# Performance work log

Hardware: AMD Instinct MI355X
Metric: run time of the kernel (lower is better)

## Reference

```python
import jax, jax.numpy as jnp
import numpy as np

B, S, D, H = 2, 2048, 1024, 16
DK = D // H

def setup_inputs() -> dict:
    key = jax.random.key(0)
    ks = jax.random.split(key, 11)
    s = 1.0 / np.sqrt(D)
    inp = {
        'q': jax.random.normal(ks[0], (B, S, D), jnp.float32),
        'k': jax.random.normal(ks[1], (B, S, D), jnp.float32),
        'v': jax.random.normal(ks[2], (B, S, D), jnp.float32),
        'mask': jnp.tril(jnp.ones((S, S), jnp.bool_))[None, None],  # [1,1,S,S] causal
        'w_q': jax.random.normal(ks[3], (D, D), jnp.float32) * s,
        'b_q': jax.random.normal(ks[4], (D,), jnp.float32) * s,
        'w_k': jax.random.normal(ks[5], (D, D), jnp.float32) * s,
        'b_k': jax.random.normal(ks[6], (D,), jnp.float32) * s,
        'w_v': jax.random.normal(ks[7], (D, D), jnp.float32) * s,
        'b_v': jax.random.normal(ks[8], (D,), jnp.float32) * s,
        'w_o': jax.random.normal(ks[9], (D, D), jnp.float32) * s,
        'b_o': jax.random.normal(ks[10], (D,), jnp.float32) * s,
    }
    return inp

def reference(q, k, v, mask, w_q, b_q, w_k, b_k, w_v, b_v, w_o, b_o):
    # Linear projections (torch Linear: x @ W^T + b)
    qh = (q @ w_q.T + b_q).reshape(B, S, H, DK).transpose(0, 2, 1, 3)  # [B,H,S,DK]
    kh = (k @ w_k.T + b_k).reshape(B, S, H, DK).transpose(0, 2, 1, 3)
    vh = (v @ w_v.T + b_v).reshape(B, S, H, DK).transpose(0, 2, 1, 3)
    scores = jnp.einsum('bhqd,bhkd->bhqk', qh, kh) / jnp.sqrt(jnp.float32(DK))
    scores = jnp.where(mask, scores, jnp.float32(-jnp.inf))
    attn = jax.nn.softmax(scores, axis=-1)  # dropout p=0.0 -> identity
    out = jnp.einsum('bhqk,bhkd->bhqd', attn, vh)
    out = out.transpose(0, 2, 1, 3).reshape(B, S, D)
    return out @ w_o.T + b_o
```

## Files before the change

### kernel.cpp

```cpp
#include <hip/hip_runtime.h>
#include <hip/hip_bf16.h>

typedef __bf16 bf16_t;
typedef __bf16 bf16x4 __attribute__((ext_vector_type(4)));
typedef __bf16 bf16x8 __attribute__((ext_vector_type(8)));
typedef float f32x4 __attribute__((ext_vector_type(4)));

#define B_ 2
#define S_ 2048
#define D_ 1024
#define H_ 16
#define DK_ 64
#define M_ (B_ * S_)

__device__ __forceinline__ f32x4 mfma16(bf16x8 a, bf16x8 b, f32x4 c) {
  return __builtin_amdgcn_mfma_f32_16x16x32_bf16(a, b, c, 0, 0, 0);
}

__device__ __forceinline__ void async_load16(const bf16_t* g, bf16_t* l) {
  __builtin_amdgcn_global_load_lds(
      (const __attribute__((address_space(1))) void*)g,
      (__attribute__((address_space(3))) void*)l, 16, 0, 0);
}


__global__ void cvt_all(const float* __restrict__ q, const float* __restrict__ k,
                        const float* __restrict__ v, const float* __restrict__ w0,
                        const float* __restrict__ w1, const float* __restrict__ w2,
                        const float* __restrict__ w3, bf16_t* __restrict__ qb,
                        bf16_t* __restrict__ kb, bf16_t* __restrict__ vb,
                        bf16_t* __restrict__ o0, bf16_t* __restrict__ o1,
                        bf16_t* __restrict__ o2, bf16_t* __restrict__ o3) {
  const int y = blockIdx.y;
  if (y >= 3 && blockIdx.x >= 512) return;
  const float* src;
  bf16_t* dst;
  float sc = 1.0f;
  switch (y) {
    case 0: src = q; dst = qb; break;
    case 1: src = k; dst = kb; break;
    case 2: src = v; dst = vb; break;
    case 3: src = w0; dst = o0; sc = 0.125f; break;
    case 4: src = w1; dst = o1; break;
    case 5: src = w2; dst = o2; break;
    default: src = w3; dst = o3; break;
  }
  long i = ((long)blockIdx.x * blockDim.x + threadIdx.x) * 8;
  const float4* s4 = (const float4*)(src + i);
  float4 a = s4[0], b = s4[1];
  bf16x8 o;
  o[0] = (bf16_t)(a.x * sc); o[1] = (bf16_t)(a.y * sc);
  o[2] = (bf16_t)(a.z * sc); o[3] = (bf16_t)(a.w * sc);
  o[4] = (bf16_t)(b.x * sc); o[5] = (bf16_t)(b.y * sc);
  o[6] = (bf16_t)(b.z * sc); o[7] = (bf16_t)(b.w * sc);
  *(bf16x8*)(dst + i) = o;
}


template <int MODE>
__device__ __forceinline__ void gemm_core(const bf16_t* __restrict__ A,
                                          const bf16_t* __restrict__ W,
                                          const float* __restrict__ bias,
                                          float bscale, void* __restrict__ Cv) {
  constexpr int N = 1024, K = 1024;
  __shared__ bf16_t As[128 * 32];
  __shared__ bf16_t Bs[128 * 32];
  const int tid = threadIdx.x;
  const int wave = tid >> 6, lane = tid & 63;
  const int quad = lane >> 4, l15 = lane & 15;
  const int wm = wave >> 1, wn = wave & 1;
  const int bm = blockIdx.y * 128, bn = blockIdx.x * 128;

  f32x4 acc[4][4] = {};

  const int srow = wave * 32 + (lane >> 2);
  const int scol = (lane & 3) * 8;
  const bf16_t* ag = A + (long)(bm + srow) * K + scol;
  const bf16_t* bg = W + (long)(bn + srow) * K + scol;
  bf16_t* asl0 = &As[(wave * 32) * 32];
  bf16_t* asl1 = &As[(wave * 32 + 16) * 32];
  bf16_t* bsl0 = &Bs[(wave * 32) * 32];
  bf16_t* bsl1 = &Bs[(wave * 32 + 16) * 32];

  for (int kk = 0; kk < K; kk += 32) {
    __syncthreads();
    async_load16(ag + kk, asl0);
    async_load16(ag + kk + 16L * K, asl1);
    async_load16(bg + kk, bsl0);
    async_load16(bg + kk + 16L * K, bsl1);
    __syncthreads();
    bf16x8 af[4], bf[4];
#pragma unroll
    for (int i = 0; i < 4; ++i)
      af[i] = *(const bf16x8*)&As[(wm * 64 + i * 16 + l15) * 32 + quad * 8];
#pragma unroll
    for (int i = 0; i < 4; ++i)
      bf[i] = *(const bf16x8*)&Bs[(wn * 64 + i * 16 + l15) * 32 + quad * 8];
#pragma unroll
    for (int mi = 0; mi < 4; ++mi)
#pragma unroll
      for (int ni = 0; ni < 4; ++ni)
        acc[mi][ni] = mfma16(af[mi], bf[ni], acc[mi][ni]);
  }

#pragma unroll
  for (int mi = 0; mi < 4; ++mi) {
#pragma unroll
    for (int ni = 0; ni < 4; ++ni) {
      const int col = bn + wn * 64 + ni * 16 + l15;
      const float bsv = bias[col] * bscale;
      f32x4 v = acc[mi][ni];
      const int row0 = bm + wm * 64 + mi * 16 + quad * 4;
      if (MODE == 3) {
        float* C = (float*)Cv;
#pragma unroll
        for (int r = 0; r < 4; ++r)
          C[(long)(row0 + r) * N + col] = v[r] + bsv;
      } else if (MODE == 1) {
        bf16_t* C = (bf16_t*)Cv;
        const int hh = col >> 6, dk = col & 63;
        const int bq = row0 >> 11, s0 = row0 & 2047;
        bf16_t* base = C + (((long)bq * H_ + hh) * S_ + s0) * DK_ + dk;
#pragma unroll
        for (int r = 0; r < 4; ++r)
          base[(long)r * DK_] = (bf16_t)(v[r] + bsv);
      } else {
        bf16_t* C = (bf16_t*)Cv;
        const int hh = col >> 6, dk = col & 63;
        const int bq = row0 >> 11, s0 = row0 & 2047;
        bf16x4 pk;
#pragma unroll
        for (int r = 0; r < 4; ++r) pk[r] = (bf16_t)(v[r] + bsv);
        *(bf16x4*)(C + (((long)bq * H_ + hh) * DK_ + dk) * S_ + s0) = pk;
      }
    }
  }
}

__global__ __launch_bounds__(256) void gemm_qkv(
    const bf16_t* __restrict__ qb, const bf16_t* __restrict__ kb,
    const bf16_t* __restrict__ vb, const bf16_t* __restrict__ wq,
    const bf16_t* __restrict__ wk, const bf16_t* __restrict__ wv,
    const float* __restrict__ biq, const float* __restrict__ bik,
    const float* __restrict__ biv, bf16_t* __restrict__ Qh,
    bf16_t* __restrict__ Kh, bf16_t* __restrict__ Vt) {
  if (blockIdx.z == 0)
    gemm_core<1>(qb, wq, biq, 0.125f, Qh);
  else if (blockIdx.z == 1)
    gemm_core<1>(kb, wk, bik, 1.0f, Kh);
  else
    gemm_core<2>(vb, wv, biv, 1.0f, Vt);
}

__global__ __launch_bounds__(256) void gemm_out64(
    const bf16_t* __restrict__ AO, const bf16_t* __restrict__ wo,
    const float* __restrict__ bo, float* __restrict__ out) {
  constexpr int N = 1024, K = 1024;
  __shared__ bf16_t As[64 * 32];
  __shared__ bf16_t Bs[128 * 32];
  const int tid = threadIdx.x;
  const int wave = tid >> 6, lane = tid & 63;
  const int quad = lane >> 4, l15 = lane & 15;
  const int wm = wave >> 1, wn = wave & 1;
  const int bm = blockIdx.y * 64, bn = blockIdx.x * 128;

  f32x4 acc[2][4] = {};

  const int srow = lane >> 2;
  const int scol = (lane & 3) * 8;
  const bf16_t* ag = AO + (long)(bm + wave * 16 + srow) * K + scol;
  const bf16_t* bg = wo + (long)(bn + wave * 32 + srow) * K + scol;
  bf16_t* asl = &As[(wave * 16) * 32];
  bf16_t* bsl0 = &Bs[(wave * 32) * 32];
  bf16_t* bsl1 = &Bs[(wave * 32 + 16) * 32];

  for (int kk = 0; kk < K; kk += 32) {
    __syncthreads();
    async_load16(ag + kk, asl);
    async_load16(bg + kk, bsl0);
    async_load16(bg + kk + 16L * K, bsl1);
    __syncthreads();
    bf16x8 af[2], bf[4];
#pragma unroll
    for (int i = 0; i < 2; ++i)
      af[i] = *(const bf16x8*)&As[(wm * 32 + i * 16 + l15) * 32 + quad * 8];
#pragma unroll
    for (int i = 0; i < 4; ++i)
      bf[i] = *(const bf16x8*)&Bs[(wn * 64 + i * 16 + l15) * 32 + quad * 8];
#pragma unroll
    for (int mi = 0; mi < 2; ++mi)
#pragma unroll
      for (int ni = 0; ni < 4; ++ni)
        acc[mi][ni] = mfma16(af[mi], bf[ni], acc[mi][ni]);
  }

#pragma unroll
  for (int mi = 0; mi < 2; ++mi) {
#pragma unroll
    for (int ni = 0; ni < 4; ++ni) {
      const int col = bn + wn * 64 + ni * 16 + l15;
      const float bsv = bo[col];
      f32x4 v = acc[mi][ni];
      const int row0 = bm + wm * 32 + mi * 16 + quad * 4;
#pragma unroll
      for (int r = 0; r < 4; ++r)
        out[(long)(row0 + r) * N + col] = v[r] + bsv;
    }
  }
}


__device__ __forceinline__ int swzK(int b) {
  return b ^ (((b >> 7) & 3) << 4) ^ (((b >> 10) & 1) << 6);
}
__device__ __forceinline__ int swzV(int b) {
  return b ^ (((b >> 7) & 7) << 4);
}

template <bool MASKED>
__device__ __forceinline__ void softmax_pa(const f32x4 st[4], float& l_i,
                                           bf16x8& pa0, bf16x8& pa1,
                                           const int qcol, const int quad) {
#pragma unroll
  for (int nb = 0; nb < 4; ++nb) {
    const int kvb = quad * 8 + (nb & 1) * 4 + (nb >> 1) * 32;
#pragma unroll
    for (int r = 0; r < 4; ++r) {
      float x = st[nb][r];
      if (MASKED && (kvb + r) > qcol) x = -30000.f;
      const float pv = __expf(x);
      l_i += pv;
      const bf16_t pb = (bf16_t)pv;
      const int idx = ((nb & 1) << 2) | r;
      if (nb < 2) pa0[idx] = pb;
      else        pa1[idx] = pb;
    }
  }
}

__global__ __launch_bounds__(256, 3) void flash_attn3(
    const bf16_t* __restrict__ Qh, const bf16_t* __restrict__ Kh,
    const bf16_t* __restrict__ Vt, bf16_t* __restrict__ Po,
    float* __restrict__ Pl) {
  const int bid = blockIdx.x;
  const int g = bid & 31;
  const int z = bid >> 5;
  const int i = z / 3, pi = z % 3;
  const int h = g & 15, b = g >> 4;
  const int tA = i, tB = 31 - i;
  const int tid = threadIdx.x, wave = tid >> 6, lane = tid & 63;
  const int quad = lane >> 4, l15 = lane & 15;
  const int qcol = wave * 16 + l15;
  const int prow = ((l15 >> 2) << 3) | (l15 & 3);

  __shared__ bf16_t Kls[2][64 * 64];
  __shared__ bf16_t Vls[2][64 * 64];

  const bf16_t* qhead = Qh + ((long)(b * H_ + h) * S_) * DK_;
  const bf16_t* khead = Kh + ((long)(b * H_ + h) * S_) * DK_;
  const bf16_t* vhead = Vt + ((long)(b * H_ + h) * DK_) * S_;

  int koffe[2], voffe[2], ldse[2];
#pragma unroll
  for (int c = 0; c < 2; ++c) {
    const int bb = c * 4096 + wave * 1024 + lane * 16;
    koffe[c] = swzK(bb) >> 1;
    const int vs = swzV(bb);
    voffe[c] = (vs >> 7) * S_ + ((vs & 127) >> 1);
    ldse[c] = c * 2048 + wave * 512;
  }

  int kro[4][2], vro[4][2];
#pragma unroll
  for (int nb = 0; nb < 4; ++nb) {
    const int krow = prow + (nb & 1) * 4 + (nb >> 1) * 32;
    const int vrow = nb * 16 + l15;
#pragma unroll
    for (int hh = 0; hh < 2; ++hh) {
      kro[nb][hh] = swzK(krow * 128 + quad * 16 + hh * 64) >> 1;
      vro[nb][hh] = swzV(vrow * 128 + quad * 16 + hh * 64) >> 1;
    }
  }

  const int qA = tA * 64 + wave * 16;
  const int qB = tB * 64 + wave * 16;
  const bf16_t* qpA = qhead + (long)(qA + l15) * DK_ + quad * 8;
  const bf16_t* qpB = qhead + (long)(qB + l15) * DK_ + quad * 8;
  const bf16x8 aqA0 = *(const bf16x8*)qpA;
  const bf16x8 aqA1 = *(const bf16x8*)(qpA + 32);
  const bf16x8 aqB0 = *(const bf16x8*)qpB;
  const bf16x8 aqB1 = *(const bf16x8*)(qpB + 32);

  f32x4 oA[4] = {}, oB[4] = {};
  float lA = 0.f, lB = 0.f;

  {
    const bf16_t* kt = khead + pi * (64 * DK_);
    const bf16_t* vt = vhead + pi * 64;
#pragma unroll
    for (int c = 0; c < 2; ++c) {
      async_load16(kt + koffe[c], &Kls[0][ldse[c]]);
      async_load16(vt + voffe[c], &Vls[0][ldse[c]]);
    }
  }

  int cur = 0;
  for (int j = pi; j <= tB; j += 3) {
    const bool pf = (j + 3 <= tB);
    if (pf) {
      const bf16_t* kt = khead + (j + 3) * (64 * DK_);
      const bf16_t* vt = vhead + (j + 3) * 64;
#pragma unroll
      for (int c = 0; c < 2; ++c) {
        async_load16(kt + koffe[c], &Kls[cur ^ 1][ldse[c]]);
        async_load16(vt + voffe[c], &Vls[cur ^ 1][ldse[c]]);
      }
      asm volatile("s_waitcnt vmcnt(4)" ::: "memory");
    } else {
      asm volatile("s_waitcnt vmcnt(0)" ::: "memory");
    }
    __builtin_amdgcn_sched_barrier(0);
    __builtin_amdgcn_s_barrier();
    __builtin_amdgcn_sched_barrier(0);

    const bf16_t* Kc = &Kls[cur][0];
    const bf16_t* Vc = &Vls[cur][0];

    bf16x8 k0[4], k1[4];
#pragma unroll
    for (int nb = 0; nb < 4; ++nb) {
      k0[nb] = *(const bf16x8*)&Kc[kro[nb][0]];
      k1[nb] = *(const bf16x8*)&Kc[kro[nb][1]];
    }

    bf16x8 paB0, paB1, paA0, paA1;
    {
      f32x4 stB[4];
#pragma unroll
      for (int nb = 0; nb < 4; ++nb) {
        f32x4 t = {};
        t = mfma16(k0[nb], aqB0, t);
        t = mfma16(k1[nb], aqB1, t);
        stB[nb] = t;
      }
      if (j == tB)
        softmax_pa<true>(stB, lB, paB0, paB1, qcol, quad);
      else
        softmax_pa<false>(stB, lB, paB0, paB1, qcol, quad);
    }
    const bool doA = (j <= tA);
    if (doA) {
      f32x4 stA[4];
#pragma unroll
      for (int nb = 0; nb < 4; ++nb) {
        f32x4 t = {};
        t = mfma16(k0[nb], aqA0, t);
        t = mfma16(k1[nb], aqA1, t);
        stA[nb] = t;
      }
      if (j == tA)
        softmax_pa<true>(stA, lA, paA0, paA1, qcol, quad);
      else
        softmax_pa<false>(stA, lA, paA0, paA1, qcol, quad);
    }

    bf16x8 v0[4], v1[4];
#pragma unroll
    for (int nb = 0; nb < 4; ++nb) {
      v0[nb] = *(const bf16x8*)&Vc[vro[nb][0]];
      v1[nb] = *(const bf16x8*)&Vc[vro[nb][1]];
    }
#pragma unroll
    for (int nb = 0; nb < 4; ++nb) {
      oB[nb] = mfma16(paB0, v0[nb], oB[nb]);
      oB[nb] = mfma16(paB1, v1[nb], oB[nb]);
    }
    if (doA) {
#pragma unroll
      for (int nb = 0; nb < 4; ++nb) {
        oA[nb] = mfma16(paA0, v0[nb], oA[nb]);
        oA[nb] = mfma16(paA1, v1[nb], oA[nb]);
      }
    }

    asm volatile("s_waitcnt lgkmcnt(0)" ::: "memory");
    __builtin_amdgcn_sched_barrier(0);
    __builtin_amdgcn_s_barrier();
    cur ^= 1;
  }

  lA += __shfl_xor(lA, 16, 64);
  lA += __shfl_xor(lA, 32, 64);
  lB += __shfl_xor(lB, 16, 64);
  lB += __shfl_xor(lB, 32, 64);

  bf16_t* po = Po + (long)pi * (M_ * D_);
  bf16_t* poA = po + (long)(b * S_ + qA + quad * 4) * D_ + h * DK_ + l15;
  bf16_t* poB = po + (long)(b * S_ + qB + quad * 4) * D_ + h * DK_ + l15;
#pragma unroll
  for (int r = 0; r < 4; ++r) {
#pragma unroll
    for (int nb = 0; nb < 4; ++nb) {
      poA[(long)r * D_ + nb * 16] = (bf16_t)oA[nb][r];
      poB[(long)r * D_ + nb * 16] = (bf16_t)oB[nb][r];
    }
  }

  if (quad == 0) {
    float* pl = Pl + (long)pi * (B_ * H_ * S_) + (long)(b * H_ + h) * S_;
    pl[qA + l15] = lA;
    pl[qB + l15] = lB;
  }
}


__global__ __launch_bounds__(256) void merge_po(const bf16_t* __restrict__ Po,
                                                const float* __restrict__ Pl,
                                                bf16_t* __restrict__ AO) {
  const long e = ((long)blockIdx.x * 256 + threadIdx.x) * 8;
  const int bs = (int)(e >> 10);
  const int d = (int)(e & 1023);
  const int h = d >> 6;
  const int b = bs >> 11, s = bs & 2047;
  const long lidx = ((long)(b * H_ + h)) * S_ + s;

  float acc[8] = {0.f, 0.f, 0.f, 0.f, 0.f, 0.f, 0.f, 0.f};
  float L = 0.f;
#pragma unroll
  for (int p = 0; p < 3; ++p) {
    bf16x8 x = *(const bf16x8*)(Po + (long)p * (M_ * D_) + e);
#pragma unroll
    for (int k = 0; k < 8; ++k) acc[k] += (float)x[k];
    L += Pl[(long)p * (B_ * H_ * S_) + lidx];
  }
  const float inv = 1.f / L;
  bf16x8 y;
#pragma unroll
  for (int k = 0; k < 8; ++k) y[k] = (bf16_t)(acc[k] * inv);
  *(bf16x8*)(AO + e) = y;
}


extern "C" void kernel_launch(void* const* d_in, const int* in_sizes, int n_in,
                              void* d_out, int out_size, void* d_ws, size_t ws_size,
                              hipStream_t stream) {
  const float* q = (const float*)d_in[0];
  const float* k = (const float*)d_in[1];
  const float* v = (const float*)d_in[2];
  const float* wq = (const float*)d_in[4];
  const float* bq = (const float*)d_in[5];
  const float* wk = (const float*)d_in[6];
  const float* bk = (const float*)d_in[7];
  const float* wv = (const float*)d_in[8];
  const float* bv = (const float*)d_in[9];
  const float* wo = (const float*)d_in[10];
  const float* bo = (const float*)d_in[11];
  float* out = (float*)d_out;

  char* ws = (char*)d_ws;
  const size_t MB = 1024 * 1024;
  bf16_t* Qh = (bf16_t*)(ws);
  bf16_t* Kh = (bf16_t*)(ws + 8 * MB);
  bf16_t* Vt = (bf16_t*)(ws + 16 * MB);
  bf16_t* AO = (bf16_t*)(ws + 24 * MB);
  bf16_t* qb = (bf16_t*)(ws + 32 * MB);
  bf16_t* kb = (bf16_t*)(ws + 40 * MB);
  bf16_t* vb = (bf16_t*)(ws + 48 * MB);
  bf16_t* wqb = (bf16_t*)(ws + 56 * MB);
  bf16_t* wkb = (bf16_t*)(ws + 58 * MB);
  bf16_t* wvb = (bf16_t*)(ws + 60 * MB);
  bf16_t* wob = (bf16_t*)(ws + 62 * MB);
  bf16_t* Po = (bf16_t*)(ws + 32 * MB);
  float* Pl = (float*)(ws + 56 * MB);

  cvt_all<<<dim3(2048, 7, 1), 256, 0, stream>>>(q, k, v, wq, wk, wv, wo, qb, kb,
                                                vb, wqb, wkb, wvb, wob);
  gemm_qkv<<<dim3(8, 32, 3), 256, 0, stream>>>(qb, kb, vb, wqb, wkb, wvb, bq, bk,
                                               bv, Qh, Kh, Vt);
  flash_attn3<<<dim3(1536, 1, 1), 256, 0, stream>>>(Qh, Kh, Vt, Po, Pl);
  merge_po<<<dim3(2048, 1, 1), 256, 0, stream>>>(Po, Pl, AO);
  gemm_out64<<<dim3(8, 64, 1), 256, 0, stream>>>(AO, wob, bo, out);
}
```

Measured before the change: 221.2 us.

## Double-buffer GEMM tiles with BK=64, swizzled LDS, and swapped grid order

Rewrites the QKV and output-projection GEMM main loops to use double-buffered LDS with a K-step of 64. The next tile is prefetched via async global-to-LDS loads while MFMAs run on the current one, and an XOR swizzle is applied to avoid LDS bank conflicts. The grid mapping is also swapped so consecutive blocks walk along M and reuse the same weight tile in cache. The change doubles LDS usage per block, which may reduce occupancy, and it relies on hand-tuned vmcnt waits.

```diff
diff --git a/kernel.cpp b/kernel.cpp
--- a/kernel.cpp
+++ b/kernel.cpp
@@ -57,50 +57,89 @@
 }
 
 
+__device__ __forceinline__ int swzG(int b) {
+  return b ^ (((b >> 7) & 7) << 4);
+}
+
+template <int NR>
+__device__ __forceinline__ void stage_tile(const bf16_t* g, bf16_t* lds,
+                                           const int* srcoff, int wave) {
+#pragma unroll
+  for (int rnd = 0; rnd < NR; ++rnd)
+    async_load16(g + srcoff[rnd], lds + rnd * 2048 + wave * 512);
+}
+
 template <int MODE>
 __device__ __forceinline__ void gemm_core(const bf16_t* __restrict__ A,
                                           const bf16_t* __restrict__ W,
                                           const float* __restrict__ bias,
                                           float bscale, void* __restrict__ Cv) {
   constexpr int N = 1024, K = 1024;
-  __shared__ bf16_t As[128 * 32];
-  __shared__ bf16_t Bs[128 * 32];
+  __shared__ bf16_t As[2][128 * 64];
+  __shared__ bf16_t Bs[2][128 * 64];
   const int tid = threadIdx.x;
   const int wave = tid >> 6, lane = tid & 63;
   const int quad = lane >> 4, l15 = lane & 15;
   const int wm = wave >> 1, wn = wave & 1;
-  const int bm = blockIdx.y * 128, bn = blockIdx.x * 128;
+  const int bm = blockIdx.x * 128, bn = blockIdx.y * 128;
 
   f32x4 acc[4][4] = {};
 
-  const int srow = wave * 32 + (lane >> 2);
-  const int scol = (lane & 3) * 8;
-  const bf16_t* ag = A + (long)(bm + srow) * K + scol;
-  const bf16_t* bg = W + (long)(bn + srow) * K + scol;
-  bf16_t* asl0 = &As[(wave * 32) * 32];
-  bf16_t* asl1 = &As[(wave * 32 + 16) * 32];
-  bf16_t* bsl0 = &Bs[(wave * 32) * 32];
-  bf16_t* bsl1 = &Bs[(wave * 32 + 16) * 32];
-
-  for (int kk = 0; kk < K; kk += 32) {
-    __syncthreads();
-    async_load16(ag + kk, asl0);
-    async_load16(ag + kk + 16L * K, asl1);
-    async_load16(bg + kk, bsl0);
-    async_load16(bg + kk + 16L * K, bsl1);
-    __syncthreads();
-    bf16x8 af[4], bf[4];
-#pragma unroll
-    for (int i = 0; i < 4; ++i)
-      af[i] = *(const bf16x8*)&As[(wm * 64 + i * 16 + l15) * 32 + quad * 8];
-#pragma unroll
-    for (int i = 0; i < 4; ++i)
-      bf[i] = *(const bf16x8*)&Bs[(wn * 64 + i * 16 + l15) * 32 + quad * 8];
-#pragma unroll
-    for (int mi = 0; mi < 4; ++mi)
-#pragma unroll
-      for (int ni = 0; ni < 4; ++ni)
-        acc[mi][ni] = mfma16(af[mi], bf[ni], acc[mi][ni]);
+  int srcoff[4];
+#pragma unroll
+  for (int rnd = 0; rnd < 4; ++rnd) {
+    const int bb = rnd * 4096 + tid * 16;
+    const int sb = swzG(bb);
+    srcoff[rnd] = (sb >> 7) * K + ((sb & 127) >> 1);
+  }
+  const bf16_t* ag = A + (long)bm * K;
+  const bf16_t* bg = W + (long)bn * K;
+
+  const int co0 = ((quad * 16) ^ ((l15 & 7) << 4)) >> 1;
+  const int co1 = ((quad * 16 + 64) ^ ((l15 & 7) << 4)) >> 1;
+  const int arow0 = (wm * 64 + l15) * 64;
+  const int brow0 = (wn * 64 + l15) * 64;
+
+  stage_tile<4>(ag, &As[0][0], srcoff, wave);
+  stage_tile<4>(bg, &Bs[0][0], srcoff, wave);
+
+  int cur = 0;
+  for (int kk = 0; kk < K; kk += 64) {
+    if (kk + 64 < K) {
+      stage_tile<4>(ag + kk + 64, &As[cur ^ 1][0], srcoff, wave);
+      stage_tile<4>(bg + kk + 64, &Bs[cur ^ 1][0], srcoff, wave);
+      asm volatile("s_waitcnt vmcnt(8)" ::: "memory");
+    } else {
+      asm volatile("s_waitcnt vmcnt(0)" ::: "memory");
+    }
+    __builtin_amdgcn_sched_barrier(0);
+    __builtin_amdgcn_s_barrier();
+    __builtin_amdgcn_sched_barrier(0);
+
+#pragma unroll
+    for (int h = 0; h < 2; ++h) {
+      const int co = h ? co1 : co0;
+      bf16x8 af[4], bfr[4];
+#pragma unroll
+      for (int i = 0; i < 4; ++i)
+        af[i] = *(const bf16x8*)&As[cur][arow0 + i * 1024 + co];
+#pragma unroll
+      for (int i = 0; i < 4; ++i)
+        bfr[i] = *(const bf16x8*)&Bs[cur][brow0 + i * 1024 + co];
+      __builtin_amdgcn_s_setprio(1);
+#pragma unroll
+      for (int mi = 0; mi < 4; ++mi)
+#pragma unroll
+        for (int ni = 0; ni < 4; ++ni)
+          acc[mi][ni] = mfma16(af[mi], bfr[ni], acc[mi][ni]);
+      __builtin_amdgcn_s_setprio(0);
+    }
+
+    asm volatile("s_waitcnt lgkmcnt(0)" ::: "memory");
+    __builtin_amdgcn_sched_barrier(0);
+    __builtin_amdgcn_s_barrier();
+    __builtin_amdgcn_sched_barrier(0);
+    cur ^= 1;
   }
 
 #pragma unroll
@@ -156,42 +195,71 @@
     const bf16_t* __restrict__ AO, const bf16_t* __restrict__ wo,
     const float* __restrict__ bo, float* __restrict__ out) {
   constexpr int N = 1024, K = 1024;
-  __shared__ bf16_t As[64 * 32];
-  __shared__ bf16_t Bs[128 * 32];
+  __shared__ bf16_t As[2][64 * 64];
+  __shared__ bf16_t Bs[2][128 * 64];
   const int tid = threadIdx.x;
   const int wave = tid >> 6, lane = tid & 63;
   const int quad = lane >> 4, l15 = lane & 15;
   const int wm = wave >> 1, wn = wave & 1;
-  const int bm = blockIdx.y * 64, bn = blockIdx.x * 128;
+  const int bm = blockIdx.x * 64, bn = blockIdx.y * 128;
 
   f32x4 acc[2][4] = {};
 
-  const int srow = lane >> 2;
-  const int scol = (lane & 3) * 8;
-  const bf16_t* ag = AO + (long)(bm + wave * 16 + srow) * K + scol;
-  const bf16_t* bg = wo + (long)(bn + wave * 32 + srow) * K + scol;
-  bf16_t* asl = &As[(wave * 16) * 32];
-  bf16_t* bsl0 = &Bs[(wave * 32) * 32];
-  bf16_t* bsl1 = &Bs[(wave * 32 + 16) * 32];
-
-  for (int kk = 0; kk < K; kk += 32) {
-    __syncthreads();
-    async_load16(ag + kk, asl);
-    async_load16(bg + kk, bsl0);
-    async_load16(bg + kk + 16L * K, bsl1);
-    __syncthreads();
-    bf16x8 af[2], bf[4];
-#pragma unroll
-    for (int i = 0; i < 2; ++i)
-      af[i] = *(const bf16x8*)&As[(wm * 32 + i * 16 + l15) * 32 + quad * 8];
-#pragma unroll
-    for (int i = 0; i < 4; ++i)
-      bf[i] = *(const bf16x8*)&Bs[(wn * 64 + i * 16 + l15) * 32 + quad * 8];
-#pragma unroll
-    for (int mi = 0; mi < 2; ++mi)
-#pragma unroll
-      for (int ni = 0; ni < 4; ++ni)
-        acc[mi][ni] = mfma16(af[mi], bf[ni], acc[mi][ni]);
+  int srcoff[4];
+#pragma unroll
+  for (int rnd = 0; rnd < 4; ++rnd) {
+    const int bb = rnd * 4096 + tid * 16;
+    const int sb = swzG(bb);
+    srcoff[rnd] = (sb >> 7) * K + ((sb & 127) >> 1);
+  }
+  const bf16_t* ag = AO + (long)bm * K;
+  const bf16_t* bg = wo + (long)bn * K;
+
+  const int co0 = ((quad * 16) ^ ((l15 & 7) << 4)) >> 1;
+  const int co1 = ((quad * 16 + 64) ^ ((l15 & 7) << 4)) >> 1;
+  const int arow0 = (wm * 32 + l15) * 64;
+  const int brow0 = (wn * 64 + l15) * 64;
+
+  stage_tile<2>(ag, &As[0][0], srcoff, wave);
+  stage_tile<4>(bg, &Bs[0][0], srcoff, wave);
+
+  int cur = 0;
+  for (int kk = 0; kk < K; kk += 64) {
+    if (kk + 64 < K) {
+      stage_tile<2>(ag + kk + 64, &As[cur ^ 1][0], srcoff, wave);
+      stage_tile<4>(bg + kk + 64, &Bs[cur ^ 1][0], srcoff, wave);
+      asm volatile("s_waitcnt vmcnt(6)" ::: "memory");
+    } else {
+      asm volatile("s_waitcnt vmcnt(0)" ::: "memory");
+    }
+    __builtin_amdgcn_sched_barrier(0);
+    __builtin_amdgcn_s_barrier();
+    __builtin_amdgcn_sched_barrier(0);
+
+#pragma unroll
+    for (int h = 0; h < 2; ++h) {
+      const int co = h ? co1 : co0;
+      bf16x8 af[2], bfr[4];
+#pragma unroll
+      for (int i = 0; i < 2; ++i)
+        af[i] = *(const bf16x8*)&As[cur][arow0 + i * 1024 + co];
+#pragma unroll
+      for (int i = 0; i < 4; ++i)
+        bfr[i] = *(const bf16x8*)&Bs[cur][brow0 + i * 1024 + co];
+      __builtin_amdgcn_s_setprio(1);
+#pragma unroll
+      for (int mi = 0; mi < 2; ++mi)
+#pragma unroll
+        for (int ni = 0; ni < 4; ++ni)
+          acc[mi][ni] = mfma16(af[mi], bfr[ni], acc[mi][ni]);
+      __builtin_amdgcn_s_setprio(0);
+    }
+
+    asm volatile("s_waitcnt lgkmcnt(0)" ::: "memory");
+    __builtin_amdgcn_sched_barrier(0);
+    __builtin_amdgcn_s_barrier();
+    __builtin_amdgcn_sched_barrier(0);
+    cur ^= 1;
   }
 
 #pragma unroll
@@ -386,6 +454,7 @@
     asm volatile("s_waitcnt lgkmcnt(0)" ::: "memory");
     __builtin_amdgcn_sched_barrier(0);
     __builtin_amdgcn_s_barrier();
+    __builtin_amdgcn_sched_barrier(0);
     cur ^= 1;
   }
 
@@ -475,9 +544,9 @@
 
   cvt_all<<<dim3(2048, 7, 1), 256, 0, stream>>>(q, k, v, wq, wk, wv, wo, qb, kb,
                                                 vb, wqb, wkb, wvb, wob);
-  gemm_qkv<<<dim3(8, 32, 3), 256, 0, stream>>>(qb, kb, vb, wqb, wkb, wvb, bq, bk,
+  gemm_qkv<<<dim3(32, 8, 3), 256, 0, stream>>>(qb, kb, vb, wqb, wkb, wvb, bq, bk,
                                                bv, Qh, Kh, Vt);
   flash_attn3<<<dim3(1536, 1, 1), 256, 0, stream>>>(Qh, Kh, Vt, Po, Pl);
   merge_po<<<dim3(2048, 1, 1), 256, 0, stream>>>(Po, Pl, AO);
-  gemm_out64<<<dim3(8, 64, 1), 256, 0, stream>>>(AO, wob, bo, out);
-}
+  gemm_out64<<<dim3(64, 8, 1), 256, 0, stream>>>(AO, wob, bo, out);
+}
```

Measured after the change: 232.8 us. +5.2%, slower.
